# Optimization experiments

Hardware: AMD Instinct MI355X
Metric: run time of the kernel (lower is better)

## Reference

```python
import jax, jax.numpy as jnp
import numpy as np

B, N, T, D, NEMB = 16, 64, 50, 4, 128  # batch, nodes, timesteps, in-dims, embed
EPS = 1e-20


def setup_inputs() -> dict:
    key = jax.random.key(0)
    ks = jax.random.split(key, 5)
    x = jax.random.normal(ks[0], (B, N, T, D), dtype=jnp.float32)
    # fully-connected directed graph without self loops: E = N*(N-1)
    send_idx, rec_idx = np.where(~np.eye(N, dtype=bool))
    eye = np.eye(N, dtype=np.float32)
    rel_send = jnp.asarray(eye[send_idx])  # [E, N] one-hot
    rel_rec = jnp.asarray(eye[rec_idx])    # [E, N] one-hot
    W_conv = jax.random.normal(ks[1], (D, NEMB), dtype=jnp.float32) / np.sqrt(D)
    b_conv = jax.random.normal(ks[2], (NEMB,), dtype=jnp.float32) * 0.01
    W_skip = jax.random.normal(ks[3], (D, NEMB), dtype=jnp.float32) / np.sqrt(D)
    b_skip = jax.random.normal(ks[4], (NEMB,), dtype=jnp.float32) * 0.01
    return dict(x=x, rel_rec=rel_rec, rel_send=rel_send,
                W_conv=W_conv, b_conv=b_conv, W_skip=W_skip, b_skip=b_skip)


def reference(x, rel_rec, rel_send, W_conv, b_conv, W_skip, b_skip):
    # gather endpoint features: [B, E, T, D]
    senders = jnp.einsum('en,bntd->betd', rel_send, x)
    receivers = jnp.einsum('en,bntd->betd', rel_rec, x)
    # per-edge inverse distance -> [B, T, E]
    spatial_norm = jnp.linalg.norm(receivers - senders, axis=-1)  # [B, E, T]
    adj_values = (1.0 / (spatial_norm + EPS)).transpose(0, 2, 1)   # [B, T, E]
    # rel_send.T @ diag(w) @ rel_rec, without the O(E^2) diag_embed: [B, T, N, N]
    adj = jnp.einsum('es,bte,er->btsr', rel_send, adj_values, rel_rec)
    # symmetric degree normalization D^{-1/2} A D^{-1/2} (no self loops)
    deg = adj.sum(-1)                      # [B, T, N]
    dinv = (deg + EPS) ** -0.5
    adj_n = dinv[..., :, None] * adj * dinv[..., None, :]
    # graph convolution branch
    xp = jnp.transpose(x, (0, 2, 1, 3))    # [B, T, N, D]
    x_conv = jnp.einsum('btnm,btmd->btnd', adj_n, xp) @ W_conv + b_conv
    x_conv = jnp.transpose(x_conv, (0, 2, 1, 3))  # [B, N, T, NEMB]
    # skip branch
    x_skip = x @ W_skip + b_skip           # [B, N, T, NEMB]
    return jax.nn.selu(jnp.concatenate([x_skip, x_conv], axis=-1))
```

## Files before the change

kernel.cpp:

```cpp
#include <hip/hip_runtime.h>
#include <hip/hip_bf16.h>

#define NB 16
#define NN 64
#define NT 50
#define ND 4
#define NE 128
#define CH 256

__device__ __forceinline__ float bf2f(unsigned short u) {
    union { unsigned int i; float f; } c;
    c.i = ((unsigned int)u) << 16;
    return c.f;
}

__device__ __forceinline__ unsigned short f2bf(float f) {
    union { float f; unsigned int i; } c;
    c.f = f;
    unsigned int x = c.i;
    x += 0x7fffu + ((x >> 16) & 1u);
    return (unsigned short)(x >> 16);
}

__device__ __forceinline__ float selu_f(float v) {
    const float scale = 1.0507009873554805f;
    const float alpha = 1.6732632423543772f;
    return v > 0.0f ? scale * v : scale * alpha * (__expf(v) - 1.0f);
}

__device__ __forceinline__ float4 ld4rt(bool isbf, const void* p, size_t off) {
    if (isbf) {
        const ushort4 v = *(const ushort4*)((const unsigned short*)p + off);
        return make_float4(bf2f(v.x), bf2f(v.y), bf2f(v.z), bf2f(v.w));
    }
    return *(const float4*)((const float*)p + off);
}

__device__ __forceinline__ void st4rt(bool isbf, void* p, size_t off, float4 r) {
    if (isbf) {
        *(ushort4*)((unsigned short*)p + off) =
            make_ushort4(f2bf(r.x), f2bf(r.y), f2bf(r.z), f2bf(r.w));
    } else {
        *(float4*)((float*)p + off) = r;
    }
}

__global__ __launch_bounds__(512) void gcn_kernel(
    const void* __restrict__ x, const void* __restrict__ rel,
    const void* __restrict__ Wc, const void* __restrict__ bc,
    const void* __restrict__ Ws, const void* __restrict__ bs,
    void* __restrict__ out)
{
    const bool isbf = (((const unsigned int*)rel)[0] != 0u);

    const int bt = blockIdx.x;
    const int b = bt / NT;
    const int t = bt - b * NT;
    const int tid = threadIdx.x;

    __shared__ float4 xt[NN];
    __shared__ float4 xsc[NN];
    __shared__ float4 y4[NN];
    __shared__ float4 Wsm[ND * NE / 4];
    __shared__ float4 Wcm[ND * NE / 4];
    __shared__ float4 bsm[NE / 4];
    __shared__ float4 bcm[NE / 4];

    if (tid < 128) {
        Wsm[tid] = ld4rt(isbf, Ws, (size_t)tid * 4);
        Wcm[tid] = ld4rt(isbf, Wc, (size_t)tid * 4);
    } else if (tid < 160) {
        const int i = tid - 128;
        bsm[i] = ld4rt(isbf, bs, (size_t)i * 4);
        bcm[i] = ld4rt(isbf, bc, (size_t)i * 4);
    } else if (tid >= 448) {
        const int nld = tid - 448;
        xt[nld] = ld4rt(isbf, x, (((size_t)b * NN + nld) * NT + t) * ND);
    }
    __syncthreads();

    const int n = tid >> 3;
    const int q = tid & 7;
    const float4 xn = xt[n];
    float av[8];
    float psum = 0.0f;
#pragma unroll
    for (int j = 0; j < 8; ++j) {
        const int m = (j << 3) + ((q + j + n) & 7);
        const float4 xm = xt[m];
        const float dx = xn.x - xm.x, dy = xn.y - xm.y;
        const float dz = xn.z - xm.z, dw = xn.w - xm.w;
        const float dist = sqrtf(dx * dx + dy * dy + dz * dz + dw * dw);
        const float v = (m == n) ? 0.0f : 1.0f / (dist + 1e-20f);
        av[j] = v;
        psum += v;
    }
    psum += __shfl_xor(psum, 1);
    psum += __shfl_xor(psum, 2);
    psum += __shfl_xor(psum, 4);
    const float di = rsqrtf(psum + 1e-20f);

    if (q == 0) {
        xsc[n] = make_float4(xn.x * di, xn.y * di, xn.z * di, xn.w * di);
    }
    __syncthreads();

    float4 acc = make_float4(0.f, 0.f, 0.f, 0.f);
#pragma unroll
    for (int j = 0; j < 8; ++j) {
        const int m = (j << 3) + ((q + j + n) & 7);
        const float w = av[j];
        const float4 xm = xsc[m];
        acc.x = fmaf(w, xm.x, acc.x);
        acc.y = fmaf(w, xm.y, acc.y);
        acc.z = fmaf(w, xm.z, acc.z);
        acc.w = fmaf(w, xm.w, acc.w);
    }
#pragma unroll
    for (int s = 1; s <= 4; s <<= 1) {
        acc.x += __shfl_xor(acc.x, s);
        acc.y += __shfl_xor(acc.y, s);
        acc.z += __shfl_xor(acc.z, s);
        acc.w += __shfl_xor(acc.w, s);
    }
    if (q == 0) {
        y4[n] = make_float4(acc.x * di, acc.y * di, acc.z * di, acc.w * di);
    }
    __syncthreads();

    const int j = tid & 63;
    const bool skipb = j < 32;
    const int jj = j & 31;
    const float4* wb = skipb ? Wsm : Wcm;
    const float4 w0 = wb[jj], w1 = wb[32 + jj], w2 = wb[64 + jj], w3 = wb[96 + jj];
    const float4 bias = skipb ? bsm[jj] : bcm[jj];
    const float4* inb = skipb ? xt : y4;
    const int w = tid >> 6;

#pragma unroll
    for (int rr = 0; rr < 8; ++rr) {
        const int nn = (rr << 3) + w;
        const float4 in = inb[nn];
        float4 r = bias;
        r.x = fmaf(in.x, w0.x, fmaf(in.y, w1.x, fmaf(in.z, w2.x, fmaf(in.w, w3.x, r.x))));
        r.y = fmaf(in.x, w0.y, fmaf(in.y, w1.y, fmaf(in.z, w2.y, fmaf(in.w, w3.y, r.y))));
        r.z = fmaf(in.x, w0.z, fmaf(in.y, w1.z, fmaf(in.z, w2.z, fmaf(in.w, w3.z, r.z))));
        r.w = fmaf(in.x, w0.w, fmaf(in.y, w1.w, fmaf(in.z, w2.w, fmaf(in.w, w3.w, r.w))));
        r.x = selu_f(r.x);
        r.y = selu_f(r.y);
        r.z = selu_f(r.z);
        r.w = selu_f(r.w);
        st4rt(isbf, out, (((size_t)b * NN + nn) * NT + t) * CH + 4 * j, r);
    }
}

extern "C" void kernel_launch(void* const* d_in, const int* in_sizes, int n_in,
                              void* d_out, int out_size, void* d_ws, size_t ws_size,
                              hipStream_t stream) {
    const void* x   = d_in[0];
    const void* rel = d_in[1];
    const void* Wc  = d_in[3];
    const void* bc  = d_in[4];
    const void* Ws  = d_in[5];
    const void* bs  = d_in[6];
    gcn_kernel<<<dim3(NB * NT), dim3(512), 0, stream>>>(x, rel, Wc, bc, Ws, bs, d_out);
}
```

Baseline: 89.72 us.

## Split each (b,t) block in half, load weights to registers, use nontemporal stores

New measurement: 90.58 us. Within noise of the previous version (+1.0%).

```diff
diff --git a/kernel.cpp b/kernel.cpp
--- a/kernel.cpp
+++ b/kernel.cpp
@@ -1,5 +1,4 @@
 #include <hip/hip_runtime.h>
-#include <hip/hip_bf16.h>
 
 #define NB 16
 #define NN 64
@@ -7,6 +6,9 @@
 #define ND 4
 #define NE 128
 #define CH 256
+
+typedef float f32x4v __attribute__((ext_vector_type(4)));
+typedef unsigned int u32x2v __attribute__((ext_vector_type(2)));
 
 __device__ __forceinline__ float bf2f(unsigned short u) {
     union { unsigned int i; float f; } c;
@@ -28,7 +30,7 @@
     return v > 0.0f ? scale * v : scale * alpha * (__expf(v) - 1.0f);
 }
 
-__device__ __forceinline__ float4 ld4rt(bool isbf, const void* p, size_t off) {
+__device__ __forceinline__ float4 ld4rt(bool isbf, const void* p, unsigned off) {
     if (isbf) {
         const ushort4 v = *(const ushort4*)((const unsigned short*)p + off);
         return make_float4(bf2f(v.x), bf2f(v.y), bf2f(v.z), bf2f(v.w));
@@ -36,16 +38,20 @@
     return *(const float4*)((const float*)p + off);
 }
 
-__device__ __forceinline__ void st4rt(bool isbf, void* p, size_t off, float4 r) {
+__device__ __forceinline__ void st4nt(bool isbf, void* p, unsigned off, float4 r) {
     if (isbf) {
-        *(ushort4*)((unsigned short*)p + off) =
-            make_ushort4(f2bf(r.x), f2bf(r.y), f2bf(r.z), f2bf(r.w));
+        u32x2v pk;
+        pk.x = ((unsigned)f2bf(r.y) << 16) | (unsigned)f2bf(r.x);
+        pk.y = ((unsigned)f2bf(r.w) << 16) | (unsigned)f2bf(r.z);
+        __builtin_nontemporal_store(pk, (u32x2v*)((unsigned short*)p + off));
     } else {
-        *(float4*)((float*)p + off) = r;
+        f32x4v v;
+        v.x = r.x; v.y = r.y; v.z = r.z; v.w = r.w;
+        __builtin_nontemporal_store(v, (f32x4v*)((float*)p + off));
     }
 }
 
-__global__ __launch_bounds__(512) void gcn_kernel(
+__global__ __launch_bounds__(256) void gcn_kernel(
     const void* __restrict__ x, const void* __restrict__ rel,
     const void* __restrict__ Wc, const void* __restrict__ bc,
     const void* __restrict__ Ws, const void* __restrict__ bs,
@@ -53,7 +59,8 @@
 {
     const bool isbf = (((const unsigned int*)rel)[0] != 0u);
 
-    const int bt = blockIdx.x;
+    const int h  = blockIdx.x & 1;
+    const int bt = blockIdx.x >> 1;
     const int b = bt / NT;
     const int t = bt - b * NT;
     const int tid = threadIdx.x;
@@ -61,43 +68,41 @@
     __shared__ float4 xt[NN];
     __shared__ float4 xsc[NN];
     __shared__ float4 y4[NN];
-    __shared__ float4 Wsm[ND * NE / 4];
-    __shared__ float4 Wcm[ND * NE / 4];
-    __shared__ float4 bsm[NE / 4];
-    __shared__ float4 bcm[NE / 4];
 
-    if (tid < 128) {
-        Wsm[tid] = ld4rt(isbf, Ws, (size_t)tid * 4);
-        Wcm[tid] = ld4rt(isbf, Wc, (size_t)tid * 4);
-    } else if (tid < 160) {
-        const int i = tid - 128;
-        bsm[i] = ld4rt(isbf, bs, (size_t)i * 4);
-        bcm[i] = ld4rt(isbf, bc, (size_t)i * 4);
-    } else if (tid >= 448) {
-        const int nld = tid - 448;
-        xt[nld] = ld4rt(isbf, x, (((size_t)b * NN + nld) * NT + t) * ND);
+    const int j = tid & 63;
+    const bool skipb = j < 32;
+    const int jj = j & 31;
+    const void* wb = skipb ? Ws : Wc;
+    const void* bb = skipb ? bs : bc;
+    const float4 w0   = ld4rt(isbf, wb, 4u * (unsigned)jj);
+    const float4 w1   = ld4rt(isbf, wb, 4u * (unsigned)(32 + jj));
+    const float4 w2   = ld4rt(isbf, wb, 4u * (unsigned)(64 + jj));
+    const float4 w3   = ld4rt(isbf, wb, 4u * (unsigned)(96 + jj));
+    const float4 bias = ld4rt(isbf, bb, 4u * (unsigned)jj);
+
+    if (tid < NN) {
+        xt[tid] = ld4rt(isbf, x, (((unsigned)b * NN + tid) * NT + t) * ND);
     }
     __syncthreads();
 
-    const int n = tid >> 3;
-    const int q = tid & 7;
+    const int n = tid >> 2;
+    const int q = tid & 3;
     const float4 xn = xt[n];
-    float av[8];
+    float av[16];
     float psum = 0.0f;
 #pragma unroll
-    for (int j = 0; j < 8; ++j) {
-        const int m = (j << 3) + ((q + j + n) & 7);
+    for (int k = 0; k < 16; ++k) {
+        const int m = (k << 2) + ((q + k + n) & 3);
         const float4 xm = xt[m];
         const float dx = xn.x - xm.x, dy = xn.y - xm.y;
         const float dz = xn.z - xm.z, dw = xn.w - xm.w;
         const float dist = sqrtf(dx * dx + dy * dy + dz * dz + dw * dw);
         const float v = (m == n) ? 0.0f : 1.0f / (dist + 1e-20f);
-        av[j] = v;
+        av[k] = v;
         psum += v;
     }
     psum += __shfl_xor(psum, 1);
     psum += __shfl_xor(psum, 2);
-    psum += __shfl_xor(psum, 4);
     const float di = rsqrtf(psum + 1e-20f);
 
     if (q == 0) {
@@ -107,9 +112,9 @@
 
     float4 acc = make_float4(0.f, 0.f, 0.f, 0.f);
 #pragma unroll
-    for (int j = 0; j < 8; ++j) {
-        const int m = (j << 3) + ((q + j + n) & 7);
-        const float w = av[j];
+    for (int k = 0; k < 16; ++k) {
+        const int m = (k << 2) + ((q + k + n) & 3);
+        const float w = av[k];
         const float4 xm = xsc[m];
         acc.x = fmaf(w, xm.x, acc.x);
         acc.y = fmaf(w, xm.y, acc.y);
@@ -117,7 +122,7 @@
         acc.w = fmaf(w, xm.w, acc.w);
     }
 #pragma unroll
-    for (int s = 1; s <= 4; s <<= 1) {
+    for (int s = 1; s <= 2; s <<= 1) {
         acc.x += __shfl_xor(acc.x, s);
         acc.y += __shfl_xor(acc.y, s);
         acc.z += __shfl_xor(acc.z, s);
@@ -128,18 +133,13 @@
     }
     __syncthreads();
 
-    const int j = tid & 63;
-    const bool skipb = j < 32;
-    const int jj = j & 31;
-    const float4* wb = skipb ? Wsm : Wcm;
-    const float4 w0 = wb[jj], w1 = wb[32 + jj], w2 = wb[64 + jj], w3 = wb[96 + jj];
-    const float4 bias = skipb ? bsm[jj] : bcm[jj];
     const float4* inb = skipb ? xt : y4;
     const int w = tid >> 6;
+    unsigned obase = (((unsigned)b * NN + 32u * h + w) * NT + t) * CH + 4u * j;
 
 #pragma unroll
     for (int rr = 0; rr < 8; ++rr) {
-        const int nn = (rr << 3) + w;
+        const int nn = 32 * h + (rr << 2) + w;
         const float4 in = inb[nn];
         float4 r = bias;
         r.x = fmaf(in.x, w0.x, fmaf(in.y, w1.x, fmaf(in.z, w2.x, fmaf(in.w, w3.x, r.x))));
@@ -150,7 +150,8 @@
         r.y = selu_f(r.y);
         r.z = selu_f(r.z);
         r.w = selu_f(r.w);
-        st4rt(isbf, out, (((size_t)b * NN + nn) * NT + t) * CH + 4 * j, r);
+        st4nt(isbf, out, obase, r);
+        obase += 4u * NT * CH;
     }
 }
 
@@ -163,5 +164,5 @@
     const void* bc  = d_in[4];
     const void* Ws  = d_in[5];
     const void* bs  = d_in[6];
-    gcn_kernel<<<dim3(NB * NT), dim3(512), 0, stream>>>(x, rel, Wc, bc, Ws, bs, d_out);
+    gcn_kernel<<<dim3(NB * NT * 2), dim3(256), 0, stream>>>(x, rel, Wc, bc, Ws, bs, d_out);
 }
```
